# Optimization experiments

Hardware: AMD Instinct MI355X
Metric: run time of the kernel (lower is better)

Reference implementation:

```python
import jax, jax.numpy as jnp
import numpy as np

B, T, C, H = 2, 2048, 1024, 16
D = C // H  # head dim = 64
EPS = 1e-5


def _layernorm(x, g, b):
    mu = jnp.mean(x, axis=-1, keepdims=True)
    var = jnp.mean((x - mu) ** 2, axis=-1, keepdims=True)
    return (x - mu) * jax.lax.rsqrt(var + EPS) * g + b


def setup_inputs() -> dict:
    key = jax.random.key(0)
    ks = jax.random.split(key, 16)
    s = 1.0 / np.sqrt(C)
    inp = {
        "x": jax.random.normal(ks[0], (B, T, C), dtype=jnp.float32),
        "Wq": jax.random.normal(ks[1], (C, C), dtype=jnp.float32) * s,
        "bq": jnp.zeros((C,), jnp.float32),
        "Wk": jax.random.normal(ks[2], (C, C), dtype=jnp.float32) * s,
        "bk": jnp.zeros((C,), jnp.float32),
        "Wv": jax.random.normal(ks[3], (C, C), dtype=jnp.float32) * s,
        "bv": jnp.zeros((C,), jnp.float32),
        "Wo": jax.random.normal(ks[4], (C, C), dtype=jnp.float32) * s,
        "bo": jnp.zeros((C,), jnp.float32),
        "ln1_g": jnp.ones((C,), jnp.float32),
        "ln1_b": jnp.zeros((C,), jnp.float32),
        "ln2_g": jnp.ones((C,), jnp.float32),
        "ln2_b": jnp.zeros((C,), jnp.float32),
        "W1": jax.random.normal(ks[5], (C, 4 * C), dtype=jnp.float32) * s,
        "b1": jnp.zeros((4 * C,), jnp.float32),
        "W2": jax.random.normal(ks[6], (4 * C, C), dtype=jnp.float32) * (1.0 / np.sqrt(4 * C)),
        "b2": jnp.zeros((C,), jnp.float32),
    }
    return inp


def _block(x, Wq, bq, Wk, bk, Wv, bv, Wo, bo, ln1_g, ln1_b, ln2_g, ln2_b, W1, b1, W2, b2):
    # --- attention sublayer (pre-LN, residual) ---
    h = _layernorm(x, ln1_g, ln1_b)
    q = (h @ Wq + bq).reshape(B, T, H, D)
    k = (h @ Wk + bk).reshape(B, T, H, D)
    v = (h @ Wv + bv).reshape(B, T, H, D)
    scores = jnp.einsum("bthd,bshd->bhts", q, k) * (1.0 / np.sqrt(D))
    attn = jax.nn.softmax(scores, axis=-1)  # dropout is identity at eval
    y = jnp.einsum("bhts,bshd->bthd", attn, v).reshape(B, T, C)
    x = x + (y @ Wo + bo)
    # --- MLP sublayer (pre-LN, residual) ---
    h2 = _layernorm(x, ln2_g, ln2_b)
    m = jax.nn.gelu(h2 @ W1 + b1, approximate=False)  # torch nn.GELU() is exact erf
    x = x + (m @ W2 + b2)
    return x


def reference(x, Wq, bq, Wk, bk, Wv, bv, Wo, bo, ln1_g, ln1_b, ln2_g, ln2_b, W1, b1, W2, b2):
    return _block(x, Wq, bq, Wk, bk, Wv, bv, Wo, bo, ln1_g, ln1_b, ln2_g, ln2_b, W1, b1, W2, b2)
```

## Files before the change

kernel.cpp:

```cpp
#include <hip/hip_runtime.h>
#include <math.h>

typedef unsigned short u16;
typedef unsigned int   u32;
using bf16x8 = __attribute__((ext_vector_type(8))) short;
using f32x4  = __attribute__((ext_vector_type(4))) float;
using f32x16 = __attribute__((ext_vector_type(16))) float;

static constexpr int Bb = 2, Tt = 2048, Cc = 1024, Hh = 16, Dd = 64;
static constexpr int QS = 3072;
static constexpr float QSCALE = 0.125f * 1.44269504089f;

__device__ __forceinline__ u16 f2bf(float f){
  u32 u = __builtin_bit_cast(u32, f);
  u += 0x7fffu + ((u >> 16) & 1u);
  return (u16)(u >> 16);
}
__device__ __forceinline__ float bf2f(u16 v){
  u32 u = (u32)v << 16;
  return __builtin_bit_cast(float, u);
}

__device__ __forceinline__ void gl2lds16(const void* g, void* l){
  __builtin_amdgcn_global_load_lds((const __attribute__((address_space(1))) void*)g,
                                   (__attribute__((address_space(3))) void*)l, 16, 0, 0);
}

template<int N> __device__ __forceinline__ void waitvm(){
  if constexpr (N == 0) asm volatile("s_waitcnt vmcnt(0)" ::: "memory");
  else if constexpr (N == 4) asm volatile("s_waitcnt vmcnt(4)" ::: "memory");
  else if constexpr (N == 6) asm volatile("s_waitcnt vmcnt(6)" ::: "memory");
  else if constexpr (N == 8) asm volatile("s_waitcnt vmcnt(8)" ::: "memory");
}

__device__ __forceinline__ void barrier_pin(){
  __builtin_amdgcn_s_barrier();
  __builtin_amdgcn_sched_barrier(0);
}

__device__ __forceinline__ f32x4 mfma16(bf16x8 a, bf16x8 b, f32x4 c){
  return __builtin_amdgcn_mfma_f32_16x16x32_bf16(a, b, c, 0, 0, 0);
}
__device__ __forceinline__ f32x16 mfma32(bf16x8 a, bf16x8 b, f32x16 c){
  return __builtin_amdgcn_mfma_f32_32x32x16_bf16(a, b, c, 0, 0, 0);
}

__device__ __forceinline__ float exp2f_fast(float x){
#if __has_builtin(__builtin_amdgcn_exp2f)
  return __builtin_amdgcn_exp2f(x);
#else
  return __expf(x * 0.69314718056f);
#endif
}

__device__ __forceinline__ float gelu_f(float x){
  return 0.5f * x * (1.0f + erff(x * 0.70710678118654752f));
}

__device__ __forceinline__ void plane_swap(u32& a, u32& b){
  asm("v_permlane32_swap_b32 %0, %1" : "+v"(a), "+v"(b));
}
__device__ __forceinline__ u32 cvtpk_bf16(float lo, float hi){
  u32 r;
  asm("v_cvt_pk_bf16_f32 %0, %1, %2" : "=v"(r) : "v"(lo), "v"(hi));
  return r;
}

__global__ __launch_bounds__(256) void ln_kernel(const float* __restrict__ x,
    const float* __restrict__ g, const float* __restrict__ b, u16* __restrict__ out)
{
  int row = blockIdx.x;
  int tid = threadIdx.x;
  const float4* xr = (const float4*)(x + (size_t)row * Cc);
  float4 v = xr[tid];
  float s  = v.x + v.y + v.z + v.w;
  float s2 = v.x*v.x + v.y*v.y + v.z*v.z + v.w*v.w;
  #pragma unroll
  for (int off = 1; off < 64; off <<= 1){ s += __shfl_xor(s, off); s2 += __shfl_xor(s2, off); }
  __shared__ float red[8];
  int wid = tid >> 6;
  if ((tid & 63) == 0){ red[wid] = s; red[4 + wid] = s2; }
  __syncthreads();
  s  = red[0] + red[1] + red[2] + red[3];
  s2 = red[4] + red[5] + red[6] + red[7];
  float mu   = s * (1.0f / Cc);
  float var  = s2 * (1.0f / Cc) - mu * mu;
  float rstd = rsqrtf(var + 1e-5f);
  const float4 gg = ((const float4*)g)[tid];
  const float4 bb = ((const float4*)b)[tid];
  ushort4 o;
  o.x = f2bf((v.x - mu) * rstd * gg.x + bb.x);
  o.y = f2bf((v.y - mu) * rstd * gg.y + bb.y);
  o.z = f2bf((v.z - mu) * rstd * gg.z + bb.z);
  o.w = f2bf((v.w - mu) * rstd * gg.w + bb.w);
  *(ushort4*)(out + (size_t)row * Cc + tid * 4) = o;
}

__global__ __launch_bounds__(256) void transpose_cast_kernel(const float* __restrict__ in,
    u16* __restrict__ out, int R, int Ccols)
{
  __shared__ float tile[32][33];
  int tx = threadIdx.x, ty = threadIdx.y;
  int c0 = blockIdx.x * 32, r0 = blockIdx.y * 32;
  #pragma unroll
  for (int j = 0; j < 4; j++) tile[ty + j*8][tx] = in[(size_t)(r0 + ty + j*8) * Ccols + c0 + tx];
  __syncthreads();
  #pragma unroll
  for (int j = 0; j < 4; j++) out[(size_t)(c0 + ty + j*8) * R + r0 + tx] = f2bf(tile[tx][ty + j*8]);
}

__global__ __launch_bounds__(256) void transpose4_kernel(
    const float* __restrict__ s0, const float* __restrict__ s1,
    const float* __restrict__ s2, const float* __restrict__ s3,
    u16* __restrict__ d0, u16* __restrict__ d1, u16* __restrict__ d2, u16* __restrict__ d3)
{
  __shared__ float tile[32][33];
  int z = blockIdx.z;
  const float* in = (z == 0) ? s0 : (z == 1) ? s1 : (z == 2) ? s2 : s3;
  u16* out        = (z == 0) ? d0 : (z == 1) ? d1 : (z == 2) ? d2 : d3;
  int tx = threadIdx.x, ty = threadIdx.y;
  int c0 = blockIdx.x * 32, r0 = blockIdx.y * 32;
  #pragma unroll
  for (int j = 0; j < 4; j++) tile[ty + j*8][tx] = in[(size_t)(r0 + ty + j*8) * 1024 + c0 + tx];
  __syncthreads();
  #pragma unroll
  for (int j = 0; j < 4; j++) out[(size_t)(c0 + ty + j*8) * 1024 + r0 + tx] = f2bf(tile[tx][ty + j*8]);
}

__global__ __launch_bounds__(256) void pack3_kernel(const float* __restrict__ a,
    const float* __restrict__ b, const float* __restrict__ c, float* __restrict__ o)
{
  int i = blockIdx.x * 256 + threadIdx.x;
  float v = (i < 1024) ? a[i] : (i < 2048 ? b[i - 1024] : c[i - 2048]);
  o[i] = v;
}

__global__ __launch_bounds__(256) void transpose_v_kernel(const u16* __restrict__ v, u16* __restrict__ vt)
{
  __shared__ u16 tile[32][33];
  int tx = threadIdx.x, ty = threadIdx.y;
  int bh = blockIdx.z; int b = bh >> 4, h = bh & 15;
  int t0 = blockIdx.x * 32, d0 = blockIdx.y * 32;
  const u16* src = v + (size_t)b * Tt * QS + h * Dd;
  #pragma unroll
  for (int j = 0; j < 4; j++) tile[ty + j*8][tx] = src[(size_t)(t0 + ty + j*8) * QS + d0 + tx];
  __syncthreads();
  u16* dst = vt + (size_t)bh * Dd * Tt;
  #pragma unroll
  for (int j = 0; j < 4; j++) dst[(size_t)(d0 + ty + j*8) * Tt + t0 + tx] = tile[tx][ty + j*8];
}

template<int BM, int BN, int WM, int WN, int WPEU, int EPI>
__global__ __launch_bounds__(WM * WN * 64, WPEU) void gemmc_kernel(
    const u16* __restrict__ A, const u16* __restrict__ BT,
    const float* __restrict__ bias, const float* __restrict__ resid,
    void* __restrict__ out, int K, int ldA, int ldOut)
{
  constexpr int THREADS = WM * WN * 64;
  constexpr int MF = (BM / WM) / 16;
  constexpr int NF = (BN / WN) / 16;
  constexpr int AG = (BM * 8) / THREADS;
  constexpr int BG = (BN * 8) / THREADS;
  constexpr int NLOADS = AG + BG;

  __shared__ alignas(16) u16 As[2][BM * 64];
  __shared__ alignas(16) u16 Bs[2][BN * 64];

  const int tid  = threadIdx.x;
  const int lane = tid & 63, wid = tid >> 6;
  const int l15  = lane & 15, lg = lane >> 4;

  const int gx  = gridDim.x;
  const int lin = blockIdx.x + gx * blockIdx.y;
  const int nwg = gx * gridDim.y;
  const int wl  = (lin & 7) * (nwg >> 3) + (lin >> 3);
  const int rowBase = (wl % gx) * BM, colBase = (wl / gx) * BN;

  const int wr = wid / WN, wc = wid % WN;

  f32x4 acc[MF][NF] = {};

  auto stage = [&](int buf, int k0){
    #pragma unroll
    for (int j = 0; j < AG; j++){
      int g = tid + THREADS * j;
      int row = g >> 3, ch = (g & 7) ^ (row & 7);
      gl2lds16(A + (size_t)(rowBase + row) * ldA + k0 + ch * 8,
               (u16*)As[buf] + (wid * 64 + THREADS * j) * 8);
    }
    #pragma unroll
    for (int j = 0; j < BG; j++){
      int g = tid + THREADS * j;
      int row = g >> 3, ch = (g & 7) ^ (row & 7);
      gl2lds16(BT + (size_t)(colBase + row) * K + k0 + ch * 8,
               (u16*)Bs[buf] + (wid * 64 + THREADS * j) * 8);
    }
  };

  stage(0, 0);
  const int nt = K >> 6;
  int cur = 0;
  for (int t = 0; t < nt; ++t, cur ^= 1){
    if (t + 1 < nt){ stage(cur ^ 1, (t + 1) << 6); waitvm<NLOADS>(); }
    else           { waitvm<0>(); }
    __builtin_amdgcn_s_barrier();
    __builtin_amdgcn_sched_barrier(0);

    const u16* Asb = (const u16*)As[cur];
    const u16* Bsb = (const u16*)Bs[cur];

    bf16x8 bfr[NF][2];
    #pragma unroll
    for (int ni = 0; ni < NF; ni++){
      int r = wc * (BN / WN) + ni * 16 + l15;
      bfr[ni][0] = *(const bf16x8*)(Bsb + r * 64 + ((lg       ^ (r & 7)) << 3));
      bfr[ni][1] = *(const bf16x8*)(Bsb + r * 64 + (((4 + lg) ^ (r & 7)) << 3));
    }
    #pragma unroll
    for (int mi = 0; mi < MF; mi++){
      int r = wr * (BM / WM) + mi * 16 + l15;
      bf16x8 a0 = *(const bf16x8*)(Asb + r * 64 + ((lg       ^ (r & 7)) << 3));
      bf16x8 a1 = *(const bf16x8*)(Asb + r * 64 + (((4 + lg) ^ (r & 7)) << 3));
      __builtin_amdgcn_s_setprio(1);
      #pragma unroll
      for (int ni = 0; ni < NF; ni++){
        acc[mi][ni] = mfma16(a0, bfr[ni][0], acc[mi][ni]);
        acc[mi][ni] = mfma16(a1, bfr[ni][1], acc[mi][ni]);
      }
      __builtin_amdgcn_s_setprio(0);
    }

    __builtin_amdgcn_sched_barrier(0);
    __builtin_amdgcn_s_barrier();
  }

  #pragma unroll
  for (int mi = 0; mi < MF; mi++){
    #pragma unroll
    for (int ni = 0; ni < NF; ni++){
      int row = rowBase + wr * (BM / WM) + mi * 16 + lg * 4;
      int col = colBase + wc * (BN / WN) + ni * 16 + l15;
      float bc = bias[col];
      #pragma unroll
      for (int r = 0; r < 4; r++){
        float val = acc[mi][ni][r] + bc;
        size_t idx = (size_t)(row + r) * ldOut + col;
        if constexpr (EPI == 0)      ((u16*)out)[idx]   = f2bf(val);
        else if constexpr (EPI == 1) ((float*)out)[idx] = val + resid[idx];
        else if constexpr (EPI == 2) ((u16*)out)[idx]   = f2bf(gelu_f(val));
        else                         ((u16*)out)[idx]   = f2bf(col < 1024 ? val * QSCALE : val);
      }
    }
  }
}

__global__ __launch_bounds__(256, 4) void attn_kernel(const u16* __restrict__ q, const u16* __restrict__ k,
    const u16* __restrict__ vt, u16* __restrict__ opart, float* __restrict__ ml)
{
  __shared__ alignas(16) u16 Ks[2][64 * 64];
  __shared__ alignas(16) u16 Vs[2][64 * 64];
  int tid  = threadIdx.x;
  int lane = tid & 63, wid = tid >> 6;
  int l31  = lane & 31, hi = lane >> 5;

  int lin = blockIdx.x + 16 * blockIdx.y;
  int wl  = (lin & 7) * 64 + (lin >> 3);
  int qt  = wl & 15, bh = wl >> 4;
  int b = bh >> 4, h = bh & 15;
  int split = blockIdx.z;
  int kt0 = split * (Tt / 2);

  int qglob = qt * 128 + wid * 32 + l31;

  const u16* qp = q + ((size_t)b * Tt + qglob) * QS + h * Dd + hi * 8;
  bf16x8 qf[4];
  #pragma unroll
  for (int s = 0; s < 4; s++) qf[s] = *(const bf16x8*)(qp + s * 16);

  const u16* kbase = k  + (size_t)b * Tt * QS + h * Dd;
  const u16* vbase = vt + (size_t)bh * Dd * Tt;

  f32x16 yacc[2] = {};
  float m2 = -1e30f, lsum = 0.f;

  int g0 = tid, g1 = tid + 256;
  int r0 = g0 >> 3, cb0 = (g0 & 7) ^ (r0 & 7);
  int r1 = g1 >> 3, cb1 = (g1 & 7) ^ (r1 & 7);

  auto stageKV = [&](int buf, int kt){
    gl2lds16(kbase + (size_t)(kt + r0) * QS + cb0 * 8, (u16*)Ks[buf] + wid * 512);
    gl2lds16(kbase + (size_t)(kt + r1) * QS + cb1 * 8, (u16*)Ks[buf] + 2048 + wid * 512);
    gl2lds16(vbase + (size_t)r0 * Tt + kt + cb0 * 8,   (u16*)Vs[buf] + wid * 512);
    gl2lds16(vbase + (size_t)r1 * Tt + kt + cb1 * 8,   (u16*)Vs[buf] + 2048 + wid * 512);
  };

  stageKV(0, kt0);
  int cur = 0;
  for (int kt = kt0; kt < kt0 + Tt / 2; kt += 64) {
    if (kt + 64 < kt0 + Tt / 2) { stageKV(cur ^ 1, kt + 64); waitvm<4>(); }
    else                        { waitvm<0>(); }
    barrier_pin();

    const u16* Ksb = (const u16*)Ks[cur];
    const u16* Vsb = (const u16*)Vs[cur];
    int rx = l31 & 7;

    f32x16 st[2] = {};
    __builtin_amdgcn_s_setprio(1);
    #pragma unroll
    for (int nb = 0; nb < 2; nb++){
      const u16* krow = Ksb + (nb * 32 + l31) * 64;
      #pragma unroll
      for (int s = 0; s < 4; s++){
        bf16x8 kf = *(const bf16x8*)(krow + (((s * 2 + hi) ^ rx) << 3));
        st[nb] = mfma32(kf, qf[s], st[nb]);
      }
    }
    __builtin_amdgcn_s_setprio(0);

    float tm[16];
    #pragma unroll
    for (int i = 0; i < 16; i++) tm[i] = fmaxf(st[0][i], st[1][i]);
    #pragma unroll
    for (int w = 8; w; w >>= 1)
      #pragma unroll
      for (int i = 0; i < w; i++) tm[i] = fmaxf(tm[i], tm[i + w]);
    u32 ma = __builtin_bit_cast(u32, tm[0]), mb = ma;
    plane_swap(ma, mb);
    float mx = fmaxf(__builtin_bit_cast(float, ma), __builtin_bit_cast(float, mb));

    float mnew = fmaxf(m2, mx);
    float alpha = exp2f_fast(m2 - mnew);
    m2 = mnew;

    #pragma unroll
    for (int nb = 0; nb < 2; nb++)
      #pragma unroll
      for (int i = 0; i < 16; i++)
        st[nb][i] = exp2f_fast(st[nb][i] - m2);

    float ts[16];
    #pragma unroll
    for (int i = 0; i < 16; i++) ts[i] = st[0][i] + st[1][i];
    #pragma unroll
    for (int w = 8; w; w >>= 1)
      #pragma unroll
      for (int i = 0; i < w; i++) ts[i] += ts[i + w];
    u32 sa = __builtin_bit_cast(u32, ts[0]), sb = sa;
    plane_swap(sa, sb);
    lsum = lsum * alpha + __builtin_bit_cast(float, sa) + __builtin_bit_cast(float, sb);

    #pragma unroll
    for (int nd = 0; nd < 2; nd++)
      #pragma unroll
      for (int i = 0; i < 16; i++) yacc[nd][i] *= alpha;

    bf16x8 pb[4];
    #pragma unroll
    for (int nb = 0; nb < 2; nb++){
      u32 c[8];
      #pragma unroll
      for (int i = 0; i < 8; i++) c[i] = cvtpk_bf16(st[nb][2 * i], st[nb][2 * i + 1]);
      plane_swap(c[0], c[2]); plane_swap(c[1], c[3]);
      plane_swap(c[4], c[6]); plane_swap(c[5], c[7]);
      u32 f0[4] = {c[0], c[1], c[2], c[3]};
      u32 f1[4] = {c[4], c[5], c[6], c[7]};
      pb[nb * 2 + 0] = *(bf16x8*)f0;
      pb[nb * 2 + 1] = *(bf16x8*)f1;
    }

    __builtin_amdgcn_s_setprio(1);
    #pragma unroll
    for (int nd = 0; nd < 2; nd++){
      const u16* vrow = Vsb + (nd * 32 + l31) * 64;
      #pragma unroll
      for (int ks = 0; ks < 4; ks++){
        bf16x8 vf = *(const bf16x8*)(vrow + (((ks * 2 + hi) ^ rx) << 3));
        yacc[nd] = mfma32(vf, pb[ks], yacc[nd]);
      }
    }
    __builtin_amdgcn_s_setprio(0);

    __builtin_amdgcn_sched_barrier(0);
    barrier_pin();
    cur ^= 1;
  }

  float inv = 1.0f / lsum;
  u16* op = opart + ((size_t)split * (Bb * Tt) + (size_t)b * Tt + qglob) * Cc + h * Dd;
  #pragma unroll
  for (int nd = 0; nd < 2; nd++){
    #pragma unroll
    for (int g = 0; g < 4; g++){
      ushort4 o;
      o.x = f2bf(yacc[nd][g * 4 + 0] * inv);
      o.y = f2bf(yacc[nd][g * 4 + 1] * inv);
      o.z = f2bf(yacc[nd][g * 4 + 2] * inv);
      o.w = f2bf(yacc[nd][g * 4 + 3] * inv);
      *(ushort4*)(op + nd * 32 + g * 8 + hi * 4) = o;
    }
  }
  if (hi == 0){
    float* mlp = ml + (((size_t)split * (Bb * Tt) + (size_t)b * Tt + qglob) * Hh + h) * 2;
    mlp[0] = m2; mlp[1] = lsum;
  }
}

__global__ __launch_bounds__(256) void combine_kernel(const u16* __restrict__ opart,
    const float* __restrict__ ml, u16* __restrict__ y)
{
  int row = blockIdx.x;
  int d0  = threadIdx.x * 4;
  int h   = d0 >> 6;
  const float* p0 = ml + ((size_t)row * Hh + h) * 2;
  const float* p1 = ml + (((size_t)(Bb * Tt) + row) * Hh + h) * 2;
  float m0 = p0[0], l0 = p0[1], m1 = p1[0], l1 = p1[1];
  float M  = fmaxf(m0, m1);
  float u0 = l0 * exp2f_fast(m0 - M), u1 = l1 * exp2f_fast(m1 - M);
  float inv = 1.0f / (u0 + u1);
  float w0 = u0 * inv, w1 = u1 * inv;
  ushort4 a = *(const ushort4*)(opart + (size_t)row * Cc + d0);
  ushort4 c = *(const ushort4*)(opart + ((size_t)(Bb * Tt) + row) * Cc + d0);
  ushort4 o;
  o.x = f2bf(bf2f(a.x) * w0 + bf2f(c.x) * w1);
  o.y = f2bf(bf2f(a.y) * w0 + bf2f(c.y) * w1);
  o.z = f2bf(bf2f(a.z) * w0 + bf2f(c.z) * w1);
  o.w = f2bf(bf2f(a.w) * w0 + bf2f(c.w) * w1);
  *(ushort4*)(y + (size_t)row * Cc + d0) = o;
}

extern "C" void kernel_launch(void* const* d_in, const int* in_sizes, int n_in,
                              void* d_out, int out_size, void* d_ws, size_t ws_size,
                              hipStream_t stream)
{
  (void)in_sizes; (void)n_in; (void)out_size; (void)ws_size;
  const float* x    = (const float*)d_in[0];
  const float* Wq   = (const float*)d_in[1];
  const float* bq   = (const float*)d_in[2];
  const float* Wk   = (const float*)d_in[3];
  const float* bk   = (const float*)d_in[4];
  const float* Wv   = (const float*)d_in[5];
  const float* bv   = (const float*)d_in[6];
  const float* Wo   = (const float*)d_in[7];
  const float* bo   = (const float*)d_in[8];
  const float* ln1g = (const float*)d_in[9];
  const float* ln1b = (const float*)d_in[10];
  const float* ln2g = (const float*)d_in[11];
  const float* ln2b = (const float*)d_in[12];
  const float* W1   = (const float*)d_in[13];
  const float* b1   = (const float*)d_in[14];
  const float* W2   = (const float*)d_in[15];
  const float* b2   = (const float*)d_in[16];

  char* ws = (char*)d_ws;
  const size_t MB = 1024 * 1024;
  u16*   wqkvt = (u16*)(ws + 0 * MB);
  u16*   wot   = (u16*)(ws + 6 * MB);
  u16*   w1t   = (u16*)(ws + 8 * MB);
  u16*   w2t   = (u16*)(ws + 16 * MB);
  float* bqkv  = (float*)(ws + 24 * MB);
  u16*   hbuf  = (u16*)(ws + 25 * MB);
  u16*   qkv   = (u16*)(ws + 33 * MB);
  u16*   vtb   = (u16*)(ws + 57 * MB);
  u16*   yb    = (u16*)(ws + 65 * MB);
  u16*   opart = (u16*)(ws + 73 * MB);
  float* x2    = (float*)(ws + 73 * MB);
  float* mlb   = (float*)(ws + 89 * MB);
  u16*   h2    = hbuf;
  u16*   mb    = qkv;

  dim3 tb(32, 8);
  transpose4_kernel<<<dim3(32, 32, 4), tb, 0, stream>>>(Wq, Wk, Wv, Wo,
      wqkvt, wqkvt + 1024 * 1024, wqkvt + 2048 * 1024, wot);
  transpose_cast_kernel<<<dim3(128, 32), tb, 0, stream>>>(W1, w1t, 1024, 4096);
  transpose_cast_kernel<<<dim3(32, 128), tb, 0, stream>>>(W2, w2t, 4096, 1024);
  pack3_kernel<<<12, 256, 0, stream>>>(bq, bk, bv, bqkv);

  ln_kernel<<<4096, 256, 0, stream>>>(x, ln1g, ln1b, hbuf);

  gemmc_kernel<128, 128, 2, 2, 2, 3><<<dim3(32, 24), 256, 0, stream>>>(hbuf, wqkvt, bqkv, nullptr, qkv, 1024, 1024, 3072);

  transpose_v_kernel<<<dim3(64, 2, 32), tb, 0, stream>>>(qkv + 2048, vtb);

  attn_kernel<<<dim3(16, 32, 2), 256, 0, stream>>>(qkv, qkv + 1024, vtb, opart, mlb);
  combine_kernel<<<4096, 256, 0, stream>>>(opart, mlb, yb);

  gemmc_kernel<64, 128, 2, 2, 3, 1><<<dim3(64, 8), 256, 0, stream>>>(yb, wot, bo, x, x2, 1024, 1024, 1024);

  ln_kernel<<<4096, 256, 0, stream>>>(x2, ln2g, ln2b, h2);

  gemmc_kernel<128, 128, 2, 2, 2, 2><<<dim3(32, 32), 256, 0, stream>>>(h2, w1t, b1, nullptr, mb, 1024, 1024, 4096);

  gemmc_kernel<64, 128, 2, 2, 3, 1><<<dim3(64, 8), 256, 0, stream>>>(mb, w2t, b2, x2, (float*)d_out, 4096, 4096, 1024);
}
```

Before: 274.3 us.

## Add 256x256 eight-wave ping-pong GEMM for QKV and MLP-up projections

Adds a new GEMM kernel with 256x256 tiles, 8 waves per block, XOR-swizzled LDS and K split into half-stages. Global-to-LDS loads for the next tile are interleaved with MFMA quarter-steps separated by barriers. The QKV and W1 GEMMs switch to it, replacing 128x128 tiles, to get more data reuse per block and overlap loads with compute. The cost is fewer blocks (192 and 256 workgroups on a GPU with many CUs), which may leave parts of the chip idle, plus more barriers per K step.

```diff
diff --git a/kernel.cpp b/kernel.cpp
--- a/kernel.cpp
+++ b/kernel.cpp
@@ -28,6 +28,7 @@
 
 template<int N> __device__ __forceinline__ void waitvm(){
   if constexpr (N == 0) asm volatile("s_waitcnt vmcnt(0)" ::: "memory");
+  else if constexpr (N == 2) asm volatile("s_waitcnt vmcnt(2)" ::: "memory");
   else if constexpr (N == 4) asm volatile("s_waitcnt vmcnt(4)" ::: "memory");
   else if constexpr (N == 6) asm volatile("s_waitcnt vmcnt(6)" ::: "memory");
   else if constexpr (N == 8) asm volatile("s_waitcnt vmcnt(8)" ::: "memory");
@@ -150,6 +151,138 @@
   for (int j = 0; j < 4; j++) dst[(size_t)(d0 + ty + j*8) * Tt + t0 + tx] = tile[tx][ty + j*8];
 }
 
+template<int EPI>
+__global__ __launch_bounds__(512, 2) void gemm8p_kernel(
+    const u16* __restrict__ A, const u16* __restrict__ BT,
+    const float* __restrict__ bias, void* __restrict__ out,
+    int K, int ldA, int ldOut)
+{
+  __shared__ alignas(16) u16 AsU[2 * 2 * 256 * 32];
+  __shared__ alignas(16) u16 BsU[2 * 2 * 256 * 32];
+
+  const int tid  = threadIdx.x;
+  const int lane = tid & 63, wid = tid >> 6;
+  const int l15  = lane & 15, lg = lane >> 4;
+
+  const int gx  = gridDim.x;
+  const int lin = blockIdx.x + gx * blockIdx.y;
+  const int nwg = gx * gridDim.y;
+  const int wl  = (lin & 7) * (nwg >> 3) + (lin >> 3);
+  const int rowBase = (wl % gx) * 256, colBase = (wl / gx) * 256;
+
+  const int wr = wid >> 2, wc = wid & 3;
+
+  f32x4 acc[8][4] = {};
+
+  auto stageH = [&](int which, int k0n, int buf){
+    const u16* src = (which & 1) ? BT : A;
+    const int  ldS = (which & 1) ? K : ldA;
+    const int  bse = (which & 1) ? colBase : rowBase;
+    const int  kh  = which >> 1;
+    u16* lds = ((which & 1) ? BsU : AsU) + buf * 16384 + kh * 8192;
+    #pragma unroll
+    for (int j = 0; j < 2; j++){
+      int s = tid + 512 * j;
+      int row = s >> 2, p = s & 3;
+      int w = p ^ ((row >> 1) & 3);
+      gl2lds16(src + (size_t)(bse + row) * ldS + k0n + kh * 32 + w * 8, lds + s * 8);
+    }
+  };
+
+  auto ldsA = [&](int buf, int kh, int pm, bf16x8* a){
+    const u16* p = AsU + buf * 16384 + kh * 8192;
+    #pragma unroll
+    for (int mi = 0; mi < 4; mi++){
+      int r = wr * 128 + pm * 64 + mi * 16 + l15;
+      a[mi] = *(const bf16x8*)(p + r * 32 + ((lg ^ ((r >> 1) & 3)) << 3));
+    }
+  };
+  auto ldsB = [&](int buf, int kh, bf16x8* b){
+    const u16* p = BsU + buf * 16384 + kh * 8192;
+    #pragma unroll
+    for (int ni = 0; ni < 4; ni++){
+      int r = wc * 64 + ni * 16 + l15;
+      b[ni] = *(const bf16x8*)(p + r * 32 + ((lg ^ ((r >> 1) & 3)) << 3));
+    }
+  };
+  auto mfmaQ = [&](int pm, const bf16x8* a, const bf16x8* b){
+    __builtin_amdgcn_s_setprio(1);
+    #pragma unroll
+    for (int mi = 0; mi < 4; mi++)
+      #pragma unroll
+      for (int ni = 0; ni < 4; ni++)
+        acc[pm * 4 + mi][ni] = mfma16(a[mi], b[ni], acc[pm * 4 + mi][ni]);
+    __builtin_amdgcn_s_setprio(0);
+  };
+
+  stageH(0, 0, 0); stageH(1, 0, 0); stageH(2, 0, 0); stageH(3, 0, 0);
+  waitvm<4>();
+  __builtin_amdgcn_s_barrier();
+
+  const int nt = K >> 6;
+  bf16x8 a[4], b[4];
+  for (int t = 0; t < nt - 1; ++t){
+    const int cur = t & 1, nxt = cur ^ 1;
+    const int kn = (t + 1) << 6;
+    ldsA(cur, 0, 0, a); ldsB(cur, 0, b); stageH(0, kn, nxt);
+    __builtin_amdgcn_s_barrier();
+    mfmaQ(0, a, b);
+    __builtin_amdgcn_s_barrier();
+    ldsA(cur, 0, 1, a); stageH(1, kn, nxt);
+    __builtin_amdgcn_s_barrier();
+    mfmaQ(1, a, b);
+    waitvm<6>();
+    __builtin_amdgcn_s_barrier();
+    ldsA(cur, 1, 0, a); ldsB(cur, 1, b); stageH(2, kn, nxt);
+    __builtin_amdgcn_s_barrier();
+    mfmaQ(0, a, b);
+    waitvm<6>();
+    __builtin_amdgcn_s_barrier();
+    ldsA(cur, 1, 1, a); stageH(3, kn, nxt);
+    __builtin_amdgcn_s_barrier();
+    mfmaQ(1, a, b);
+    waitvm<4>();
+    __builtin_amdgcn_s_barrier();
+  }
+  {
+    const int cur = (nt - 1) & 1;
+    ldsA(cur, 0, 0, a); ldsB(cur, 0, b);
+    __builtin_amdgcn_s_barrier();
+    mfmaQ(0, a, b);
+    __builtin_amdgcn_s_barrier();
+    ldsA(cur, 0, 1, a);
+    __builtin_amdgcn_s_barrier();
+    mfmaQ(1, a, b);
+    waitvm<2>();
+    __builtin_amdgcn_s_barrier();
+    ldsA(cur, 1, 0, a); ldsB(cur, 1, b);
+    __builtin_amdgcn_s_barrier();
+    mfmaQ(0, a, b);
+    waitvm<0>();
+    __builtin_amdgcn_s_barrier();
+    ldsA(cur, 1, 1, a);
+    __builtin_amdgcn_s_barrier();
+    mfmaQ(1, a, b);
+  }
+
+  #pragma unroll
+  for (int mi = 0; mi < 8; mi++){
+    #pragma unroll
+    for (int ni = 0; ni < 4; ni++){
+      int row = rowBase + wr * 128 + mi * 16 + lg * 4;
+      int col = colBase + wc * 64 + ni * 16 + l15;
+      float bc = bias[col];
+      #pragma unroll
+      for (int r = 0; r < 4; r++){
+        float val = acc[mi][ni][r] + bc;
+        size_t idx = (size_t)(row + r) * ldOut + col;
+        if constexpr (EPI == 2) ((u16*)out)[idx] = f2bf(gelu_f(val));
+        else                    ((u16*)out)[idx] = f2bf(col < 1024 ? val * QSCALE : val);
+      }
+    }
+  }
+}
+
 template<int BM, int BN, int WM, int WN, int WPEU, int EPI>
 __global__ __launch_bounds__(WM * WN * 64, WPEU) void gemmc_kernel(
     const u16* __restrict__ A, const u16* __restrict__ BT,
@@ -245,10 +378,8 @@
       for (int r = 0; r < 4; r++){
         float val = acc[mi][ni][r] + bc;
         size_t idx = (size_t)(row + r) * ldOut + col;
-        if constexpr (EPI == 0)      ((u16*)out)[idx]   = f2bf(val);
-        else if constexpr (EPI == 1) ((float*)out)[idx] = val + resid[idx];
-        else if constexpr (EPI == 2) ((u16*)out)[idx]   = f2bf(gelu_f(val));
-        else                         ((u16*)out)[idx]   = f2bf(col < 1024 ? val * QSCALE : val);
+        if constexpr (EPI == 1) ((float*)out)[idx] = val + resid[idx];
+        else                    ((u16*)out)[idx]   = f2bf(val);
       }
     }
   }
@@ -478,7 +609,7 @@
 
   ln_kernel<<<4096, 256, 0, stream>>>(x, ln1g, ln1b, hbuf);
 
-  gemmc_kernel<128, 128, 2, 2, 2, 3><<<dim3(32, 24), 256, 0, stream>>>(hbuf, wqkvt, bqkv, nullptr, qkv, 1024, 1024, 3072);
+  gemm8p_kernel<3><<<dim3(16, 12), 512, 0, stream>>>(hbuf, wqkvt, bqkv, qkv, 1024, 1024, 3072);
 
   transpose_v_kernel<<<dim3(64, 2, 32), tb, 0, stream>>>(qkv + 2048, vtb);
 
@@ -489,7 +620,7 @@
 
   ln_kernel<<<4096, 256, 0, stream>>>(x2, ln2g, ln2b, h2);
 
-  gemmc_kernel<128, 128, 2, 2, 2, 2><<<dim3(32, 32), 256, 0, stream>>>(h2, w1t, b1, nullptr, mb, 1024, 1024, 4096);
+  gemm8p_kernel<2><<<dim3(16, 16), 512, 0, stream>>>(h2, w1t, b1, mb, 1024, 1024, 4096);
 
   gemmc_kernel<64, 128, 2, 2, 3, 1><<<dim3(64, 8), 256, 0, stream>>>(mb, w2t, b2, x2, (float*)d_out, 4096, 4096, 1024);
 }
```

Result: faster. 268.2 us (-2.2%).
